# Performance work log

Measured on AMD Instinct MI355X. Metric: run time of the kernel, lower is better.

## Reference

```python
import jax, jax.numpy as jnp
import numpy as np

HIDDEN = 2048
NUM_HEADS = 16
HEAD_DIM = 128
WINDOW = 1024
ROPE_THETA = 10000.0
B, L = 1, 4096


def setup_inputs() -> dict:
    key = jax.random.key(0)
    k0, k1, k2, k3, k4 = jax.random.split(key, 5)
    s = 1.0 / np.sqrt(HIDDEN)
    return {
        "hidden_states": jax.random.normal(k0, (B, L, HIDDEN), dtype=jnp.float32),
        "wq": jax.random.normal(k1, (HIDDEN, NUM_HEADS * HEAD_DIM), dtype=jnp.float32) * s,
        "wk": jax.random.normal(k2, (HIDDEN, NUM_HEADS * HEAD_DIM), dtype=jnp.float32) * s,
        "wv": jax.random.normal(k3, (HIDDEN, NUM_HEADS * HEAD_DIM), dtype=jnp.float32) * s,
        "wo": jax.random.normal(k4, (NUM_HEADS * HEAD_DIM, HIDDEN), dtype=jnp.float32) * s,
    }


def _apply_rotary(x, cos, sin):
    # x: [B, H, L, D]; cos/sin: [L, D/2]
    d2 = x.shape[-1] // 2
    x1, x2 = x[..., :d2], x[..., d2:]
    return jnp.concatenate([x1 * cos - x2 * sin, x2 * cos + x1 * sin], axis=-1)


def reference(hidden_states, wq, wk, wv, wo):
    Bsz, Ln, _ = hidden_states.shape
    dtype = hidden_states.dtype
    scale = HEAD_DIM ** (-0.5)

    def split_heads(x):
        return x.reshape(Bsz, Ln, NUM_HEADS, HEAD_DIM).transpose(0, 2, 1, 3)

    q = split_heads(hidden_states @ wq)
    k = split_heads(hidden_states @ wk)
    v = split_heads(hidden_states @ wv)

    inv_freq = 1.0 / (ROPE_THETA ** (jnp.arange(0, HEAD_DIM, 2, dtype=jnp.float32) / HEAD_DIM))
    pos = jnp.arange(Ln, dtype=jnp.float32)
    freqs = pos[:, None] * inv_freq[None, :]  # [L, D/2]
    cos = jnp.cos(freqs).astype(dtype)
    sin = jnp.sin(freqs).astype(dtype)

    q = _apply_rotary(q, cos, sin)
    k = _apply_rotary(k, cos, sin)

    q_pos = jnp.arange(Ln)[:, None]
    k_pos = jnp.arange(Ln)[None, :]
    valid = (k_pos > q_pos - WINDOW) & (k_pos <= q_pos)  # [L, L]
    neg = jnp.finfo(dtype).min

    attn = jnp.einsum("bhqd,bhkd->bhqk", q, k) * scale
    attn = jnp.where(valid, attn, neg)
    attn = jax.nn.softmax(attn, axis=-1)
    out = jnp.einsum("bhqk,bhkd->bhqd", attn, v)
    out = out.transpose(0, 2, 1, 3).reshape(Bsz, Ln, NUM_HEADS * HEAD_DIM)
    return out @ wo
```

## Files before the change

### kernel.cpp

```cpp
#include <hip/hip_runtime.h>
#include <cstdint>
#include <cstddef>

typedef unsigned short u16;
typedef __bf16 bf16x8 __attribute__((ext_vector_type(8)));
typedef float f32x4 __attribute__((ext_vector_type(4)));
typedef unsigned short u16x8 __attribute__((ext_vector_type(8)));

#define SEQ 4096
#define HID 2048
#define NH 16
#define HD 128
#define WIN 1024

__device__ __forceinline__ float bf2f(u16 u) {
  union { unsigned int i; float f; } v; v.i = ((unsigned int)u) << 16; return v.f;
}
__device__ __forceinline__ u16 f2bf(float f) {
  union { float f; unsigned int i; } v; v.f = f;
  unsigned int r = v.i + 0x7FFFu + ((v.i >> 16) & 1u);
  return (u16)(r >> 16);
}
__device__ __forceinline__ u16 f2bf_rne(float f) {
  union { __bf16 b; u16 u; } v; v.b = (__bf16)f; return v.u;
}
__device__ __forceinline__ unsigned pk2(float lo, float hi) {
  return (unsigned)f2bf_rne(lo) | ((unsigned)f2bf_rne(hi) << 16);
}
__device__ __forceinline__ float exp2a(float x) {
  float r; asm("v_exp_f32 %0, %1" : "=v"(r) : "v"(x)); return r;
}
template<int L2R>
__device__ __forceinline__ unsigned swz(unsigned o) { return o ^ (((o >> L2R) & 7u) << 4); }

__device__ __forceinline__ void gload_lds16(const u16* g, u16* l) {
  __builtin_amdgcn_global_load_lds((const __attribute__((address_space(1))) void*)g,
                                   (__attribute__((address_space(3))) void*)l, 16, 0, 0);
}


__global__ void cast_f32_bf16(const float* __restrict__ in, u16* __restrict__ out, int n4) {
  int i = blockIdx.x * blockDim.x + threadIdx.x;
  if (i < n4) {
    float4 v = ((const float4*)in)[i];
    union { u16 u[4]; unsigned long long ll; } r;
    r.u[0] = f2bf(v.x); r.u[1] = f2bf(v.y); r.u[2] = f2bf(v.z); r.u[3] = f2bf(v.w);
    ((unsigned long long*)out)[i] = r.ll;
  }
}

__global__ void transpose_cast4(const float* __restrict__ w0, const float* __restrict__ w1,
                                const float* __restrict__ w2, const float* __restrict__ w3,
                                u16* __restrict__ o0, u16* __restrict__ o1,
                                u16* __restrict__ o2, u16* __restrict__ o3) {
  __shared__ float t[32][33];
  const float* W = (blockIdx.z == 0) ? w0 : (blockIdx.z == 1) ? w1 : (blockIdx.z == 2) ? w2 : w3;
  u16* Wt = (blockIdx.z == 0) ? o0 : (blockIdx.z == 1) ? o1 : (blockIdx.z == 2) ? o2 : o3;
  const int tx = threadIdx.x & 31, ty = threadIdx.x >> 5;
  const int x0 = blockIdx.x * 32, y0 = blockIdx.y * 32;
#pragma unroll
  for (int i = 0; i < 4; ++i)
    t[ty + i * 8][tx] = W[(size_t)(y0 + ty + i * 8) * HID + x0 + tx];
  __syncthreads();
#pragma unroll
  for (int i = 0; i < 4; ++i)
    Wt[(size_t)(x0 + ty + i * 8) * HID + y0 + tx] = f2bf(t[tx][ty + i * 8]);
}

__global__ void rope_table(float* __restrict__ ctab, float* __restrict__ stab) {
  int idx = blockIdx.x * blockDim.x + threadIdx.x;
  int pos = idx >> 6, i = idx & 63;
  float invf = expf(-(float)i * 0.14391156831212787f);
  float ang = (float)pos * invf;
  float s, c;
  sincosf(ang, &s, &c);
  ctab[idx] = c; stab[idx] = s;
}


__global__ __launch_bounds__(256, 2) void gemm_qkv_kernel(
    const u16* __restrict__ X, const u16* __restrict__ Wqt, const u16* __restrict__ Wkt,
    const u16* __restrict__ Wvt, u16* __restrict__ Qo, u16* __restrict__ Ko, u16* __restrict__ Vo,
    const float* __restrict__ ctab, const float* __restrict__ stab) {
  __shared__ u16 ldsA[2][8192];
  __shared__ u16 ldsB[2][8192];
  int flat = (blockIdx.z * 32 + blockIdx.y) * 16 + blockIdx.x;
  int nf = (flat & 7) * 192 + (flat >> 3);
  int bx = nf & 15, by = (nf >> 4) & 31, bz = nf >> 9;
  const u16* Bt = (bz == 0) ? Wqt : (bz == 1) ? Wkt : Wvt;
  u16* Cp = (bz == 0) ? Qo : (bz == 1) ? Ko : Vo;
  const int brow = by * 128, bcol = bx * 128;

  const int lane = threadIdx.x & 63;
  const int wv = threadIdx.x >> 6;
  const int g = lane >> 4, c = lane & 15;
  const int K = HID, N = HID;

  const f32x4 zero = {0.f, 0.f, 0.f, 0.f};
  f32x4 acc[2][8];
#pragma unroll
  for (int m = 0; m < 2; ++m)
#pragma unroll
    for (int n = 0; n < 8; ++n) acc[m][n] = zero;

  auto stage = [&](int buf, int kt) {
    const int k0 = kt * 64;
#pragma unroll
    for (int i = 0; i < 4; ++i) {
      unsigned o = ((unsigned)(wv * 4 + i) * 64 + (unsigned)lane) * 16u;
      unsigned r = o >> 7;
      unsigned cb = swz<7>(o) & 127u;
      const size_t gcol = (size_t)k0 + (cb >> 1);
      gload_lds16(X + (size_t)(brow + r) * K + gcol, &ldsA[buf][(wv * 4 + i) * 512]);
      gload_lds16(Bt + (size_t)(bcol + r) * K + gcol, &ldsB[buf][(wv * 4 + i) * 512]);
    }
  };

  stage(0, 0);
  __syncthreads();
  int buf = 0;
  const int nt = K / 64;
  for (int kt = 0; kt < nt; ++kt) {
    if (kt + 1 < nt) stage(buf ^ 1, kt + 1);
    __builtin_amdgcn_s_setprio(1);
#pragma unroll
    for (int s = 0; s < 2; ++s) {
      const unsigned kb = (unsigned)(s * 64 + g * 16);
      bf16x8 af[2], bfv[8];
#pragma unroll
      for (int m = 0; m < 2; ++m) {
        unsigned row = wv * 32 + m * 16 + c;
        af[m] = *(const bf16x8*)((const char*)&ldsA[buf][0] + swz<7>(row * 128 + kb));
      }
#pragma unroll
      for (int n = 0; n < 8; ++n) {
        unsigned row = n * 16 + c;
        bfv[n] = *(const bf16x8*)((const char*)&ldsB[buf][0] + swz<7>(row * 128 + kb));
      }
#pragma unroll
      for (int m = 0; m < 2; ++m)
#pragma unroll
        for (int n = 0; n < 8; ++n)
          acc[m][n] = __builtin_amdgcn_mfma_f32_16x16x32_bf16(af[m], bfv[n], acc[m][n], 0, 0, 0);
    }
    __builtin_amdgcn_s_setprio(0);
    __syncthreads();
    buf ^= 1;
  }

  if (bz < 2) {
#pragma unroll
    for (int m = 0; m < 2; ++m) {
      const int rbase = brow + wv * 32 + m * 16 + g * 4;
#pragma unroll
      for (int r = 0; r < 4; ++r) {
        const int pos = rbase + r;
        const float* cp = ctab + (size_t)pos * 64;
        const float* sp = stab + (size_t)pos * 64;
        u16* crow = Cp + (size_t)pos * N + bcol;
#pragma unroll
        for (int n = 0; n < 4; ++n) {
          const int i = n * 16 + c;
          const float x1 = acc[m][n][r], x2 = acc[m][n + 4][r];
          const float co = cp[i], si = sp[i];
          crow[i] = f2bf(x1 * co - x2 * si);
          crow[i + 64] = f2bf(x2 * co + x1 * si);
        }
      }
    }
  } else {
#pragma unroll
    for (int m = 0; m < 2; ++m) {
      const int rbase = brow + wv * 32 + m * 16 + g * 4;
#pragma unroll
      for (int r = 0; r < 4; ++r) {
        u16* crow = Cp + (size_t)(rbase + r) * N + bcol;
#pragma unroll
        for (int n = 0; n < 8; ++n)
          crow[n * 16 + c] = f2bf(acc[m][n][r]);
      }
    }
  }
}


__global__ __launch_bounds__(256, 2) void gemm_out_kernel(
    const u16* __restrict__ Ob, const u16* __restrict__ Wot, float* __restrict__ out) {
  __shared__ u16 ldsA[2][8192];
  __shared__ u16 ldsB[2][8192];
  int flat = blockIdx.y * 16 + blockIdx.x;
  int nf = (flat & 7) * 64 + (flat >> 3);
  int bx = nf & 15, by = nf >> 4;
  const int brow = by * 128, bcol = bx * 128;

  const int lane = threadIdx.x & 63;
  const int wv = threadIdx.x >> 6;
  const int wr = wv >> 1, wc = wv & 1;
  const int g = lane >> 4, c = lane & 15;
  const int K = HID, N = HID;

  const f32x4 zero = {0.f, 0.f, 0.f, 0.f};
  f32x4 acc[4][4];
#pragma unroll
  for (int m = 0; m < 4; ++m)
#pragma unroll
    for (int n = 0; n < 4; ++n) acc[m][n] = zero;

  auto stage = [&](int buf, int kt) {
    const int k0 = kt * 64;
#pragma unroll
    for (int i = 0; i < 4; ++i) {
      unsigned o = ((unsigned)(wv * 4 + i) * 64 + (unsigned)lane) * 16u;
      unsigned r = o >> 7;
      unsigned cb = swz<7>(o) & 127u;
      const size_t gcol = (size_t)k0 + (cb >> 1);
      gload_lds16(Ob + (size_t)(brow + r) * K + gcol, &ldsA[buf][(wv * 4 + i) * 512]);
      gload_lds16(Wot + (size_t)(bcol + r) * K + gcol, &ldsB[buf][(wv * 4 + i) * 512]);
    }
  };

  stage(0, 0);
  __syncthreads();
  int buf = 0;
  const int nt = K / 64;
  for (int kt = 0; kt < nt; ++kt) {
    if (kt + 1 < nt) stage(buf ^ 1, kt + 1);
    __builtin_amdgcn_s_setprio(1);
#pragma unroll
    for (int s = 0; s < 2; ++s) {
      const unsigned kb = (unsigned)(s * 64 + g * 16);
      bf16x8 af[4], bfv[4];
#pragma unroll
      for (int m = 0; m < 4; ++m) {
        unsigned row = wr * 64 + m * 16 + c;
        af[m] = *(const bf16x8*)((const char*)&ldsA[buf][0] + swz<7>(row * 128 + kb));
      }
#pragma unroll
      for (int n = 0; n < 4; ++n) {
        unsigned row = wc * 64 + n * 16 + c;
        bfv[n] = *(const bf16x8*)((const char*)&ldsB[buf][0] + swz<7>(row * 128 + kb));
      }
#pragma unroll
      for (int m = 0; m < 4; ++m)
#pragma unroll
        for (int n = 0; n < 4; ++n)
          acc[m][n] = __builtin_amdgcn_mfma_f32_16x16x32_bf16(af[m], bfv[n], acc[m][n], 0, 0, 0);
    }
    __builtin_amdgcn_s_setprio(0);
    __syncthreads();
    buf ^= 1;
  }

#pragma unroll
  for (int m = 0; m < 4; ++m) {
    const int rbase = brow + wr * 64 + m * 16 + g * 4;
#pragma unroll
    for (int n = 0; n < 4; ++n) {
      const int cbase = bcol + wc * 64 + n * 16 + c;
#pragma unroll
      for (int r = 0; r < 4; ++r)
        out[(size_t)(rbase + r) * N + cbase] = acc[m][n][r];
    }
  }
}


__global__ __launch_bounds__(256, 3) void attn_kernel(
    const u16* __restrict__ Q, const u16* __restrict__ K,
    const u16* __restrict__ V, u16* __restrict__ O) {
  __shared__ u16 k_lds[2][8192];
  __shared__ u16 vt_lds[8192];

  const int lane = threadIdx.x & 63;
  const int wv = threadIdx.x >> 6;
  const int g = lane >> 4;
  const int c = lane & 15;

  int flat = blockIdx.y * 64 + blockIdx.x;
  int nf = (flat & 7) * 128 + (flat >> 3);
  const int q0 = (nf & 63) * 64;
  const int h = nf >> 6;
  const int qw = q0 + wv * 16;
  const int qpos = qw + c;

#pragma unroll
  for (int i = 0; i < 4; ++i) {
    unsigned o = ((unsigned)(wv * 4 + i) * 64 + (unsigned)lane) * 16u;
    unsigned r = o >> 8;
    unsigned cb = swz<8>(o) & 255u;
    gload_lds16(Q + (size_t)(q0 + r) * HID + h * HD + (cb >> 1), &k_lds[0][(wv * 4 + i) * 512]);
  }
  __syncthreads();
  bf16x8 qf[4];
#pragma unroll
  for (int s = 0; s < 4; ++s) {
    unsigned row = wv * 16 + c;
    qf[s] = *(const bf16x8*)((const char*)&k_lds[0][0] + swz<8>(row * 256 + s * 64 + g * 16));
  }
  __syncthreads();

  auto stageK = [&](int buf, int t0) {
#pragma unroll
    for (int i = 0; i < 4; ++i) {
      unsigned o = ((unsigned)(wv * 4 + i) * 64 + (unsigned)lane) * 16u;
      unsigned r = o >> 8;
      unsigned key = (r & 0x23u) | ((r & 0x0Cu) << 1) | ((r & 0x10u) >> 2);
      unsigned cb = swz<8>(o) & 255u;
      gload_lds16(K + (size_t)(t0 + (int)key) * HID + h * HD + (cb >> 1),
                  &k_lds[buf][(wv * 4 + i) * 512]);
    }
  };
  u16x8 vr[4];
  auto loadV = [&](int t0) {
    const u16x8* src = (const u16x8*)(V + (size_t)(t0 + lane) * HID + h * HD + wv * 32);
#pragma unroll
    for (int it = 0; it < 4; ++it) vr[it] = src[it];
  };
  auto writeVT = [&]() {
#pragma unroll
    for (int it = 0; it < 4; ++it)
#pragma unroll
      for (int j = 0; j < 8; ++j) {
        const int d = wv * 32 + it * 8 + j;
        vt_lds[d * 64 + (lane ^ ((d & 7) << 3))] = vr[it][j];
      }
  };

  const int t_start = (q0 >= WIN) ? (q0 - WIN) : 0;

  loadV(t_start);
  stageK(0, t_start);
  __syncthreads();
  writeVT();
  __syncthreads();

  const f32x4 zero = {0.f, 0.f, 0.f, 0.f};
  float mrow = -1e30f, lrow = 0.f;
  f32x4 oacc[8];
#pragma unroll
  for (int d = 0; d < 8; ++d) oacc[d] = zero;

  const float scale2 = 0.12751743f;
  int b = 0;

  for (int t0 = t_start; t0 <= q0; t0 += 64) {
    const bool has_next = (t0 + 64 <= q0);
    if (has_next) {
      loadV(t0 + 64);
      stageK(b ^ 1, t0 + 64);
    }

    f32x4 sa[4];
#pragma unroll
    for (int kf = 0; kf < 4; ++kf) sa[kf] = zero;
    __builtin_amdgcn_s_setprio(1);
#pragma unroll
    for (int s = 0; s < 4; ++s) {
#pragma unroll
      for (int kf = 0; kf < 4; ++kf) {
        unsigned row = kf * 16 + c;
        bf16x8 kb = *(const bf16x8*)((const char*)&k_lds[b][0] + swz<8>(row * 256 + s * 64 + g * 16));
        sa[kf] = __builtin_amdgcn_mfma_f32_16x16x32_bf16(kb, qf[s], sa[kf], 0, 0, 0);
      }
    }
    __builtin_amdgcn_s_setprio(0);

    const bool diag = (t0 == q0);
    const bool lowm = (q0 >= WIN) && (t0 == t_start);
    if (diag) {
#pragma unroll
      for (int kf = 0; kf < 4; ++kf) {
        const int kbase = t0 + (kf >> 1) * 32 + g * 8 + (kf & 1) * 4;
#pragma unroll
        for (int r = 0; r < 4; ++r) {
          float x = sa[kf][r] * scale2;
          sa[kf][r] = (kbase + r <= qpos) ? x : -1e30f;
        }
      }
    } else if (lowm) {
#pragma unroll
      for (int kf = 0; kf < 4; ++kf) {
        const int kbase = t0 + (kf >> 1) * 32 + g * 8 + (kf & 1) * 4;
#pragma unroll
        for (int r = 0; r < 4; ++r) {
          float x = sa[kf][r] * scale2;
          sa[kf][r] = (kbase + r > qpos - WIN) ? x : -1e30f;
        }
      }
    } else {
#pragma unroll
      for (int kf = 0; kf < 4; ++kf)
#pragma unroll
        for (int r = 0; r < 4; ++r) sa[kf][r] *= scale2;
    }

    float tmax = -3e38f;
#pragma unroll
    for (int kf = 0; kf < 4; ++kf)
#pragma unroll
      for (int r = 0; r < 4; ++r) tmax = fmaxf(tmax, sa[kf][r]);
    tmax = fmaxf(tmax, __shfl_xor(tmax, 16));
    tmax = fmaxf(tmax, __shfl_xor(tmax, 32));

    if (!__all((int)(tmax <= mrow + 8.f))) {
      const float mn = fmaxf(mrow, tmax);
      const float al = exp2a(mrow - mn);
      mrow = mn;
      lrow *= al;
      float alo[4];
#pragma unroll
      for (int r = 0; r < 4; ++r) alo[r] = __shfl(al, (lane & 48) | (g * 4 + r));
#pragma unroll
      for (int df = 0; df < 8; ++df)
#pragma unroll
        for (int r = 0; r < 4; ++r) oacc[df][r] *= alo[r];
    }

    float rs = 0.f;
    if (diag || lowm) {
#pragma unroll
      for (int kf = 0; kf < 4; ++kf)
#pragma unroll
        for (int r = 0; r < 4; ++r) {
          const float x = sa[kf][r];
          const float p = (x < -1e29f) ? 0.f : exp2a(x - mrow);
          sa[kf][r] = p; rs += p;
        }
    } else {
#pragma unroll
      for (int kf = 0; kf < 4; ++kf)
#pragma unroll
        for (int r = 0; r < 4; ++r) {
          const float p = exp2a(sa[kf][r] - mrow);
          sa[kf][r] = p; rs += p;
        }
    }
    rs += __shfl_xor(rs, 16);
    rs += __shfl_xor(rs, 32);
    lrow += rs;

    union { bf16x8 v; unsigned u[4]; } pa0, pa1;
    pa0.u[0] = pk2(sa[0][0], sa[0][1]); pa0.u[1] = pk2(sa[0][2], sa[0][3]);
    pa0.u[2] = pk2(sa[1][0], sa[1][1]); pa0.u[3] = pk2(sa[1][2], sa[1][3]);
    pa1.u[0] = pk2(sa[2][0], sa[2][1]); pa1.u[1] = pk2(sa[2][2], sa[2][3]);
    pa1.u[2] = pk2(sa[3][0], sa[3][1]); pa1.u[3] = pk2(sa[3][2], sa[3][3]);

    __builtin_amdgcn_s_setprio(1);
#pragma unroll
    for (int s2 = 0; s2 < 2; ++s2) {
      const bf16x8 pa = s2 ? pa1.v : pa0.v;
#pragma unroll
      for (int df = 0; df < 8; ++df) {
        const int row = df * 16 + c;
        const bf16x8 vb = *(const bf16x8*)&vt_lds[row * 64 + ((s2 * 32 + g * 8) ^ ((row & 7) << 3))];
        oacc[df] = __builtin_amdgcn_mfma_f32_16x16x32_bf16(pa, vb, oacc[df], 0, 0, 0);
      }
    }
    __builtin_amdgcn_s_setprio(0);

    asm volatile("s_waitcnt lgkmcnt(0)" ::: "memory");
    __builtin_amdgcn_s_barrier();

    if (has_next) {
      asm volatile("s_waitcnt vmcnt(4)" ::: "memory");
      writeVT();
    }
    asm volatile("s_waitcnt vmcnt(0) lgkmcnt(0)" ::: "memory");
    __builtin_amdgcn_s_barrier();
    b ^= 1;
  }

  float ilo[4];
  const float invl = 1.f / lrow;
#pragma unroll
  for (int r = 0; r < 4; ++r) ilo[r] = __shfl(invl, (lane & 48) | (g * 4 + r));
#pragma unroll
  for (int df = 0; df < 8; ++df)
#pragma unroll
    for (int r = 0; r < 4; ++r) {
      const int row = qw + g * 4 + r;
      const int col = h * HD + df * 16 + c;
      O[(size_t)row * HID + col] = f2bf(oacc[df][r] * ilo[r]);
    }
}


extern "C" void kernel_launch(void* const* d_in, const int* in_sizes, int n_in,
                              void* d_out, int out_size, void* d_ws, size_t ws_size,
                              hipStream_t stream) {
  const float* hidden = (const float*)d_in[0];
  const float* wq = (const float*)d_in[1];
  const float* wk = (const float*)d_in[2];
  const float* wv = (const float*)d_in[3];
  const float* wo = (const float*)d_in[4];
  float* out = (float*)d_out;

  char* ws = (char*)d_ws;
  u16* Xb  = (u16*)ws;                 ws += (size_t)SEQ * HID * 2;
  u16* Wqt = (u16*)ws;                 ws += (size_t)HID * HID * 2;
  u16* Wkt = (u16*)ws;                 ws += (size_t)HID * HID * 2;
  u16* Wvt = (u16*)ws;                 ws += (size_t)HID * HID * 2;
  u16* Wot = (u16*)ws;                 ws += (size_t)HID * HID * 2;
  u16* Qb  = (u16*)ws;                 ws += (size_t)SEQ * HID * 2;
  u16* Kb  = (u16*)ws;                 ws += (size_t)SEQ * HID * 2;
  u16* Vb  = (u16*)ws;                 ws += (size_t)SEQ * HID * 2;
  u16* Ob  = (u16*)ws;                 ws += (size_t)SEQ * HID * 2;
  float* ctab = (float*)ws;            ws += (size_t)SEQ * 64 * 4;
  float* stab = (float*)ws;            ws += (size_t)SEQ * 64 * 4;

  cast_f32_bf16<<<(SEQ * HID / 4 + 255) / 256, 256, 0, stream>>>(hidden, Xb, SEQ * HID / 4);

  dim3 tg(64, 64, 4);
  transpose_cast4<<<tg, 256, 0, stream>>>(wq, wk, wv, wo, Wqt, Wkt, Wvt, Wot);

  rope_table<<<(SEQ * 64) / 256, 256, 0, stream>>>(ctab, stab);

  dim3 gq(HID / 128, SEQ / 128, 3);
  gemm_qkv_kernel<<<gq, 256, 0, stream>>>(Xb, Wqt, Wkt, Wvt, Qb, Kb, Vb, ctab, stab);

  dim3 ga(SEQ / 64, NH);
  attn_kernel<<<ga, 256, 0, stream>>>(Qb, Kb, Vb, Ob);

  dim3 go(HID / 128, SEQ / 128);
  gemm_out_kernel<<<go, 256, 0, stream>>>(Ob, Wot, out);
}
```

Measured before the change: 265.2 us.

## Unify GEMMs with 8-wave blocks and 4-stage LDS pipeline with vmcnt waits

Both projection GEMMs now share one templated body that runs 512 threads (8 waves) per 128x128 tile. It uses a 4-deep LDS ring buffer prefetched three tiles ahead, with explicit vmcnt waits and a single barrier per k-step instead of double buffering with two syncs. Each wave now owns a 32x64 subtile, and the B column mapping keeps RoPE pairs inside one wave. The aim is to hide global-load latency and raise the number of waves issuing MFMA. The cost is 128KB of LDS per block, which may limit occupancy to one block per CU despite the launch bounds.

```diff
diff --git a/kernel.cpp b/kernel.cpp
--- a/kernel.cpp
+++ b/kernel.cpp
@@ -78,190 +78,147 @@
 }
 
 
-__global__ __launch_bounds__(256, 2) void gemm_qkv_kernel(
+template<bool OUT_F32, bool ROPE>
+__device__ __forceinline__ void gemm_body(const u16* __restrict__ A, const u16* __restrict__ Bt,
+                                          void* __restrict__ C, int brow, int bcol, bool do_rope,
+                                          const float* __restrict__ ctab,
+                                          const float* __restrict__ stab,
+                                          u16 (&ldsA)[4][8192], u16 (&ldsB)[4][8192]) {
+  const int tid = threadIdx.x;
+  const int lane = tid & 63;
+  const int wv = tid >> 6;
+  const int wr = wv >> 1;
+  const int wc = wv & 1;
+  const int g = lane >> 4, c = lane & 15;
+  const int K = HID, N = HID;
+  const int nmap0 = 2 * wc;
+
+  const f32x4 zero = {0.f, 0.f, 0.f, 0.f};
+  f32x4 acc[2][4];
+#pragma unroll
+  for (int m = 0; m < 2; ++m)
+#pragma unroll
+    for (int j = 0; j < 4; ++j) acc[m][j] = zero;
+
+  auto stage = [&](int buf, int kt) {
+    const int k0 = kt * 64;
+#pragma unroll
+    for (int i = 0; i < 2; ++i) {
+      unsigned idx = (unsigned)(i * 512 + tid);
+      unsigned o = idx * 16u;
+      unsigned r = o >> 7;
+      unsigned cb = swz<7>(o) & 127u;
+      const size_t gcol = (size_t)k0 + (cb >> 1);
+      gload_lds16(A + (size_t)(brow + r) * K + gcol, &ldsA[buf][idx * 8]);
+      gload_lds16(Bt + (size_t)(bcol + r) * K + gcol, &ldsB[buf][idx * 8]);
+    }
+  };
+
+  const int nt = K / 64;
+  stage(0, 0); stage(1, 1); stage(2, 2);
+
+  int bc = 0;
+  for (int kt = 0; kt < nt; ++kt) {
+    if (kt + 2 < nt)       asm volatile("s_waitcnt vmcnt(8)" ::: "memory");
+    else if (kt + 1 < nt)  asm volatile("s_waitcnt vmcnt(4)" ::: "memory");
+    else                   asm volatile("s_waitcnt vmcnt(0)" ::: "memory");
+    asm volatile("s_waitcnt lgkmcnt(0)" ::: "memory");
+    __builtin_amdgcn_s_barrier();
+    asm volatile("" ::: "memory");
+    __builtin_amdgcn_sched_barrier(0);
+
+    if (kt + 3 < nt) {
+      int bs = bc + 3; if (bs >= 4) bs -= 4;
+      stage(bs, kt + 3);
+    }
+
+    __builtin_amdgcn_s_setprio(1);
+#pragma unroll
+    for (int s = 0; s < 2; ++s) {
+      const unsigned kb = (unsigned)(s * 64 + g * 16);
+      bf16x8 af[2], bfv[4];
+#pragma unroll
+      for (int m = 0; m < 2; ++m) {
+        unsigned row = (unsigned)(wr * 32 + m * 16 + c);
+        af[m] = *(const bf16x8*)((const char*)&ldsA[bc][0] + swz<7>(row * 128 + kb));
+      }
+#pragma unroll
+      for (int j = 0; j < 4; ++j) {
+        const int n = nmap0 + ((j & 1) ? 1 : 0) + ((j >> 1) ? 4 : 0);
+        unsigned row = (unsigned)(n * 16 + c);
+        bfv[j] = *(const bf16x8*)((const char*)&ldsB[bc][0] + swz<7>(row * 128 + kb));
+      }
+#pragma unroll
+      for (int m = 0; m < 2; ++m)
+#pragma unroll
+        for (int j = 0; j < 4; ++j)
+          acc[m][j] = __builtin_amdgcn_mfma_f32_16x16x32_bf16(af[m], bfv[j], acc[m][j], 0, 0, 0);
+    }
+    __builtin_amdgcn_s_setprio(0);
+
+    ++bc; if (bc == 4) bc = 0;
+  }
+
+  if (ROPE && do_rope) {
+#pragma unroll
+    for (int m = 0; m < 2; ++m) {
+      const int rbase = brow + wr * 32 + m * 16 + g * 4;
+#pragma unroll
+      for (int r = 0; r < 4; ++r) {
+        const int pos = rbase + r;
+        const float* cp = ctab + (size_t)pos * 64;
+        const float* sp = stab + (size_t)pos * 64;
+        u16* crow = (u16*)C + (size_t)pos * N + bcol;
+#pragma unroll
+        for (int jj = 0; jj < 2; ++jj) {
+          const int i = wc * 32 + jj * 16 + c;
+          const float x1 = acc[m][jj][r], x2 = acc[m][jj + 2][r];
+          const float co = cp[i], si = sp[i];
+          crow[i] = f2bf(x1 * co - x2 * si);
+          crow[i + 64] = f2bf(x2 * co + x1 * si);
+        }
+      }
+    }
+  } else {
+#pragma unroll
+    for (int m = 0; m < 2; ++m) {
+      const int rbase = brow + wr * 32 + m * 16 + g * 4;
+#pragma unroll
+      for (int r = 0; r < 4; ++r) {
+#pragma unroll
+        for (int j = 0; j < 4; ++j) {
+          const int n = nmap0 + (j & 1) + ((j >> 1) ? 4 : 0);
+          const size_t idx = (size_t)(rbase + r) * N + bcol + n * 16 + c;
+          if (OUT_F32) ((float*)C)[idx] = acc[m][j][r];
+          else ((u16*)C)[idx] = f2bf(acc[m][j][r]);
+        }
+      }
+    }
+  }
+}
+
+__global__ __launch_bounds__(512, 2) void gemm_qkv_kernel(
     const u16* __restrict__ X, const u16* __restrict__ Wqt, const u16* __restrict__ Wkt,
     const u16* __restrict__ Wvt, u16* __restrict__ Qo, u16* __restrict__ Ko, u16* __restrict__ Vo,
     const float* __restrict__ ctab, const float* __restrict__ stab) {
-  __shared__ u16 ldsA[2][8192];
-  __shared__ u16 ldsB[2][8192];
+  __shared__ u16 ldsA[4][8192];
+  __shared__ u16 ldsB[4][8192];
   int flat = (blockIdx.z * 32 + blockIdx.y) * 16 + blockIdx.x;
   int nf = (flat & 7) * 192 + (flat >> 3);
   int bx = nf & 15, by = (nf >> 4) & 31, bz = nf >> 9;
   const u16* Bt = (bz == 0) ? Wqt : (bz == 1) ? Wkt : Wvt;
   u16* Cp = (bz == 0) ? Qo : (bz == 1) ? Ko : Vo;
-  const int brow = by * 128, bcol = bx * 128;
-
-  const int lane = threadIdx.x & 63;
-  const int wv = threadIdx.x >> 6;
-  const int g = lane >> 4, c = lane & 15;
-  const int K = HID, N = HID;
-
-  const f32x4 zero = {0.f, 0.f, 0.f, 0.f};
-  f32x4 acc[2][8];
-#pragma unroll
-  for (int m = 0; m < 2; ++m)
-#pragma unroll
-    for (int n = 0; n < 8; ++n) acc[m][n] = zero;
-
-  auto stage = [&](int buf, int kt) {
-    const int k0 = kt * 64;
-#pragma unroll
-    for (int i = 0; i < 4; ++i) {
-      unsigned o = ((unsigned)(wv * 4 + i) * 64 + (unsigned)lane) * 16u;
-      unsigned r = o >> 7;
-      unsigned cb = swz<7>(o) & 127u;
-      const size_t gcol = (size_t)k0 + (cb >> 1);
-      gload_lds16(X + (size_t)(brow + r) * K + gcol, &ldsA[buf][(wv * 4 + i) * 512]);
-      gload_lds16(Bt + (size_t)(bcol + r) * K + gcol, &ldsB[buf][(wv * 4 + i) * 512]);
-    }
-  };
-
-  stage(0, 0);
-  __syncthreads();
-  int buf = 0;
-  const int nt = K / 64;
-  for (int kt = 0; kt < nt; ++kt) {
-    if (kt + 1 < nt) stage(buf ^ 1, kt + 1);
-    __builtin_amdgcn_s_setprio(1);
-#pragma unroll
-    for (int s = 0; s < 2; ++s) {
-      const unsigned kb = (unsigned)(s * 64 + g * 16);
-      bf16x8 af[2], bfv[8];
-#pragma unroll
-      for (int m = 0; m < 2; ++m) {
-        unsigned row = wv * 32 + m * 16 + c;
-        af[m] = *(const bf16x8*)((const char*)&ldsA[buf][0] + swz<7>(row * 128 + kb));
-      }
-#pragma unroll
-      for (int n = 0; n < 8; ++n) {
-        unsigned row = n * 16 + c;
-        bfv[n] = *(const bf16x8*)((const char*)&ldsB[buf][0] + swz<7>(row * 128 + kb));
-      }
-#pragma unroll
-      for (int m = 0; m < 2; ++m)
-#pragma unroll
-        for (int n = 0; n < 8; ++n)
-          acc[m][n] = __builtin_amdgcn_mfma_f32_16x16x32_bf16(af[m], bfv[n], acc[m][n], 0, 0, 0);
-    }
-    __builtin_amdgcn_s_setprio(0);
-    __syncthreads();
-    buf ^= 1;
-  }
-
-  if (bz < 2) {
-#pragma unroll
-    for (int m = 0; m < 2; ++m) {
-      const int rbase = brow + wv * 32 + m * 16 + g * 4;
-#pragma unroll
-      for (int r = 0; r < 4; ++r) {
-        const int pos = rbase + r;
-        const float* cp = ctab + (size_t)pos * 64;
-        const float* sp = stab + (size_t)pos * 64;
-        u16* crow = Cp + (size_t)pos * N + bcol;
-#pragma unroll
-        for (int n = 0; n < 4; ++n) {
-          const int i = n * 16 + c;
-          const float x1 = acc[m][n][r], x2 = acc[m][n + 4][r];
-          const float co = cp[i], si = sp[i];
-          crow[i] = f2bf(x1 * co - x2 * si);
-          crow[i + 64] = f2bf(x2 * co + x1 * si);
-        }
-      }
-    }
-  } else {
-#pragma unroll
-    for (int m = 0; m < 2; ++m) {
-      const int rbase = brow + wv * 32 + m * 16 + g * 4;
-#pragma unroll
-      for (int r = 0; r < 4; ++r) {
-        u16* crow = Cp + (size_t)(rbase + r) * N + bcol;
-#pragma unroll
-        for (int n = 0; n < 8; ++n)
-          crow[n * 16 + c] = f2bf(acc[m][n][r]);
-      }
-    }
-  }
-}
-
-
-__global__ __launch_bounds__(256, 2) void gemm_out_kernel(
+  gemm_body<false, true>(X, Bt, Cp, by * 128, bx * 128, bz < 2, ctab, stab, ldsA, ldsB);
+}
+
+__global__ __launch_bounds__(512, 2) void gemm_out_kernel(
     const u16* __restrict__ Ob, const u16* __restrict__ Wot, float* __restrict__ out) {
-  __shared__ u16 ldsA[2][8192];
-  __shared__ u16 ldsB[2][8192];
+  __shared__ u16 ldsA[4][8192];
+  __shared__ u16 ldsB[4][8192];
   int flat = blockIdx.y * 16 + blockIdx.x;
   int nf = (flat & 7) * 64 + (flat >> 3);
   int bx = nf & 15, by = nf >> 4;
-  const int brow = by * 128, bcol = bx * 128;
-
-  const int lane = threadIdx.x & 63;
-  const int wv = threadIdx.x >> 6;
-  const int wr = wv >> 1, wc = wv & 1;
-  const int g = lane >> 4, c = lane & 15;
-  const int K = HID, N = HID;
-
-  const f32x4 zero = {0.f, 0.f, 0.f, 0.f};
-  f32x4 acc[4][4];
-#pragma unroll
-  for (int m = 0; m < 4; ++m)
-#pragma unroll
-    for (int n = 0; n < 4; ++n) acc[m][n] = zero;
-
-  auto stage = [&](int buf, int kt) {
-    const int k0 = kt * 64;
-#pragma unroll
-    for (int i = 0; i < 4; ++i) {
-      unsigned o = ((unsigned)(wv * 4 + i) * 64 + (unsigned)lane) * 16u;
-      unsigned r = o >> 7;
-      unsigned cb = swz<7>(o) & 127u;
-      const size_t gcol = (size_t)k0 + (cb >> 1);
-      gload_lds16(Ob + (size_t)(brow + r) * K + gcol, &ldsA[buf][(wv * 4 + i) * 512]);
-      gload_lds16(Wot + (size_t)(bcol + r) * K + gcol, &ldsB[buf][(wv * 4 + i) * 512]);
-    }
-  };
-
-  stage(0, 0);
-  __syncthreads();
-  int buf = 0;
-  const int nt = K / 64;
-  for (int kt = 0; kt < nt; ++kt) {
-    if (kt + 1 < nt) stage(buf ^ 1, kt + 1);
-    __builtin_amdgcn_s_setprio(1);
-#pragma unroll
-    for (int s = 0; s < 2; ++s) {
-      const unsigned kb = (unsigned)(s * 64 + g * 16);
-      bf16x8 af[4], bfv[4];
-#pragma unroll
-      for (int m = 0; m < 4; ++m) {
-        unsigned row = wr * 64 + m * 16 + c;
-        af[m] = *(const bf16x8*)((const char*)&ldsA[buf][0] + swz<7>(row * 128 + kb));
-      }
-#pragma unroll
-      for (int n = 0; n < 4; ++n) {
-        unsigned row = wc * 64 + n * 16 + c;
-        bfv[n] = *(const bf16x8*)((const char*)&ldsB[buf][0] + swz<7>(row * 128 + kb));
-      }
-#pragma unroll
-      for (int m = 0; m < 4; ++m)
-#pragma unroll
-        for (int n = 0; n < 4; ++n)
-          acc[m][n] = __builtin_amdgcn_mfma_f32_16x16x32_bf16(af[m], bfv[n], acc[m][n], 0, 0, 0);
-    }
-    __builtin_amdgcn_s_setprio(0);
-    __syncthreads();
-    buf ^= 1;
-  }
-
-#pragma unroll
-  for (int m = 0; m < 4; ++m) {
-    const int rbase = brow + wr * 64 + m * 16 + g * 4;
-#pragma unroll
-    for (int n = 0; n < 4; ++n) {
-      const int cbase = bcol + wc * 64 + n * 16 + c;
-#pragma unroll
-      for (int r = 0; r < 4; ++r)
-        out[(size_t)(rbase + r) * N + cbase] = acc[m][n][r];
-    }
-  }
+  gemm_body<true, false>(Ob, Wot, out, by * 128, bx * 128, false, nullptr, nullptr, ldsA, ldsB);
 }
 
 
@@ -516,11 +473,11 @@
   rope_table<<<(SEQ * 64) / 256, 256, 0, stream>>>(ctab, stab);
 
   dim3 gq(HID / 128, SEQ / 128, 3);
-  gemm_qkv_kernel<<<gq, 256, 0, stream>>>(Xb, Wqt, Wkt, Wvt, Qb, Kb, Vb, ctab, stab);
+  gemm_qkv_kernel<<<gq, 512, 0, stream>>>(Xb, Wqt, Wkt, Wvt, Qb, Kb, Vb, ctab, stab);
 
   dim3 ga(SEQ / 64, NH);
   attn_kernel<<<ga, 256, 0, stream>>>(Qb, Kb, Vb, Ob);
 
   dim3 go(HID / 128, SEQ / 128);
-  gemm_out_kernel<<<go, 256, 0, stream>>>(Ob, Wot, out);
-}
+  gemm_out_kernel<<<go, 512, 0, stream>>>(Ob, Wot, out);
+}
```

After: 360.6 us. 1.36x slower.
